# Kernel optimization log

Measured on AMD Instinct MI355X. Metric: run time of the kernel, lower is better.

## Reference

```python
import jax, jax.numpy as jnp
import numpy as np

HEADS = 8
DIM_HEAD = 64
QUERY_DIM = 320
INNER = HEADS * DIM_HEAD
B = 1
N = 2304          # 48*48 latent pixels
HS = WS = 48
SCALE = DIM_HEAD ** -0.5
ATTN_MATRIX_SCALE = 1.5   # injection_config['T']


def setup_inputs() -> dict:
    key = jax.random.key(0)
    ks = jax.random.split(key, 10)
    f = lambda k, s: jax.random.normal(k, s, dtype=jnp.float32)
    return {
        'x': f(ks[0], (B, N, QUERY_DIM)),
        'Wq': f(ks[1], (QUERY_DIM, INNER)) * 0.05,
        'Wo': f(ks[2], (INNER, QUERY_DIM)) * 0.05,
        'bo': jnp.zeros((QUERY_DIM,), jnp.float32),
        'q_injected': f(ks[3], (B * HEADS, N, DIM_HEAD)),
        'k_injected': f(ks[4], (B * HEADS, N, DIM_HEAD)),
        'v_injected': f(ks[5], (B * HEADS, N, DIM_HEAD)),
        'cnt_k_injected': f(ks[6], (B * HEADS, N, DIM_HEAD)),
        'cnt_v_injected': f(ks[7], (B * HEADS, N, DIM_HEAD)),
        'mask': jax.random.uniform(ks[8], (HS, WS), dtype=jnp.float32),
    }


def _split_heads(t):
    # 'b n (h d) -> (b h) n d'
    b, n, _ = t.shape
    return t.reshape(b, n, HEADS, DIM_HEAD).transpose(0, 2, 1, 3).reshape(b * HEADS, n, DIM_HEAD)


def reference(x, Wq, Wo, bo, q_injected, k_injected, v_injected,
              cnt_k_injected, cnt_v_injected, mask):
    # --- q/k/v with injection (b=1 so torch.cat([.]*b) is identity) ---
    q_in = q_injected                          # (bh, N, d)
    q_ = _split_heads(x @ Wq)                  # to_q(x) -> (bh, N, d)
    q = 0.5 * q_in + 0.5 * q_                  # blended query
    k = k_injected
    v = v_injected
    q_cnt, k_cnt, v_cnt = q_in, cnt_k_injected, cnt_v_injected

    # --- get_batch_sim: content-content similarity (b=1 => rearrange is identity) ---
    cc_sim = jnp.einsum('hid,hjd->hij', q_cnt, k_cnt) * SCALE     # (h, N, N)

    # --- get_batch_sim_with_mask ---
    sim = jnp.einsum('hid,hjd->hij', q, k) * (ATTN_MATRIX_SCALE * SCALE)  # (h, N, N)
    sim_r = sim.reshape(HEADS, HS, WS, N)
    cc_r = cc_sim.reshape(HEADS, HS, WS, N)
    max_sim = jnp.einsum('hid,hjd->hij', q_cnt, k)                # delta_q x delta_k (=self.k)
    max_sim_r = max_sim.reshape(HEADS, HS, WS, N)
    min_cc = jnp.min(cc_r, axis=3, keepdims=True)                 # (h, HS, WS, 1)
    max_ms = jnp.max(max_sim_r, axis=3, keepdims=True)            # (h, HS, WS, 1)

    # binary-threshold the mask, flip sign, bilinear-resize to (HS, WS)
    m = jnp.where(mask < 0.5, -1.0, jnp.where(mask > 0.5, 1.0, mask)) * -1.0
    m = jax.image.resize(m[None, None], (1, 1, HS, WS), method='bilinear')
    m = m.reshape(1, HS, WS, 1)

    gvm = (min_cc - max_ms) * m                                   # gradual_vanished_mask
    sim = (sim_r + gvm).reshape(HEADS, N, N)                      # rows [:WS] == all rows here

    # B=1 => the view/permute/reshape block is identity: sim, cc_sim are (h, N, N)
    # concatenated softmax over style keys and content keys
    cat_sim = jnp.concatenate([sim, cc_sim], axis=2)              # (h, N, 2N)
    cat_attn = jax.nn.softmax(cat_sim, axis=-1)
    cat_v = jnp.concatenate([v, v_cnt], axis=1)                   # (h, 2N, d)
    cat_out = jnp.einsum('hij,hjd->hid', cat_attn, cat_v)         # (h, N, d)

    # 'h (b n) d -> b n (h d)' with b=1
    out = cat_out.transpose(1, 0, 2).reshape(B, N, INNER)
    return out @ Wo + bo
```

## Files before the change

### kernel.cpp

```cpp
#include <hip/hip_runtime.h>
#include <math.h>

#define HEADS 8
#define NTOK  2304
#define DH    64
#define QD    320
#define INNER 512
#define NSPLIT 4
#define TPS   18
#define PSTR  68

typedef _Float16 f16;
typedef f16  f16x4 __attribute__((ext_vector_type(4)));
typedef f16  f16x8 __attribute__((ext_vector_type(8)));
typedef float f32x4 __attribute__((ext_vector_type(4)));

#define MFMA(a,b,c) __builtin_amdgcn_mfma_f32_16x16x32_f16((a),(b),(c),0,0,0)

#define GLDS(gp, lp) __builtin_amdgcn_global_load_lds(                      \
    (const __attribute__((address_space(1))) void*)(gp),                    \
    (__attribute__((address_space(3))) void*)(lp), 16, 0, 0)

#if __has_builtin(__builtin_amdgcn_exp2f)
#define EXP2(x) __builtin_amdgcn_exp2f(x)
#else
#define EXP2(x) exp2f(x)
#endif

#define LOG2E 1.44269504f

static __device__ __forceinline__ unsigned pkrtz(float a, float b) {
#if __has_builtin(__builtin_amdgcn_cvt_pkrtz)
  return __builtin_bit_cast(unsigned, __builtin_amdgcn_cvt_pkrtz(a, b));
#else
  union { f16 h[2]; unsigned u; } c;
  c.h[0] = (f16)a; c.h[1] = (f16)b;
  return c.u;
#endif
}

__global__ __launch_bounds__(256) void prep_all(
    const float* __restrict__ qi, const float* __restrict__ ki,
    const float* __restrict__ kc, const float* __restrict__ x,
    const float* __restrict__ v,  const float* __restrict__ vc,
    const float* __restrict__ Wq, const float* __restrict__ Wo,
    f16* __restrict__ oq, f16* __restrict__ ok, f16* __restrict__ okc,
    f16* __restrict__ ox, f16* __restrict__ vt, f16* __restrict__ vct,
    f16* __restrict__ WqT, f16* __restrict__ WoT)
{
  __shared__ float T[64][65];
  const int bid = blockIdx.x;
  const int tid = threadIdx.x;

  if (bid < 2088) {
    int i = bid * 256 + tid;
    const float* src; f16* dst; float s = 1.0f; int off;
    if (i < 147456)      { src = qi; dst = oq;  off = i; }
    else if (i < 294912) { src = ki; dst = ok;  off = i - 147456; }
    else if (i < 442368) { src = kc; dst = okc; off = i - 294912; s = 0.125f * LOG2E; }
    else                 { src = x;  dst = ox;  off = i - 442368; }
    float4 a = reinterpret_cast<const float4*>(src)[off * 2];
    float4 b = reinterpret_cast<const float4*>(src)[off * 2 + 1];
    f16x8 o;
    o[0] = (f16)(a.x * s); o[1] = (f16)(a.y * s);
    o[2] = (f16)(a.z * s); o[3] = (f16)(a.w * s);
    o[4] = (f16)(b.x * s); o[5] = (f16)(b.y * s);
    o[6] = (f16)(b.z * s); o[7] = (f16)(b.w * s);
    *reinterpret_cast<f16x8*>(&dst[(size_t)off * 8]) = o;
  } else if (bid < 2664) {
    int t = bid - 2088;
    int z = t / 288, rem = t % 288;
    int h = rem / 36, nt = rem % 36;
    const float* src = z ? vc : v;
    f16* dst = z ? vct : vt;
    const int n0 = nt * 64;
    const size_t base = ((size_t)h * NTOK + n0) * DH;
    for (int it = 0; it < 4; ++it) {
      int idx = tid + it * 256;
      int n = idx >> 4, d0 = (idx & 15) * 4;
      float4 a = *reinterpret_cast<const float4*>(&src[base + (size_t)n * DH + d0]);
      T[n][d0] = a.x; T[n][d0 + 1] = a.y; T[n][d0 + 2] = a.z; T[n][d0 + 3] = a.w;
    }
    __syncthreads();
    for (int it = 0; it < 2; ++it) {
      int idx = tid + it * 256;
      int d = idx >> 3, c0 = (idx & 7) * 8;
      f16x8 o;
      #pragma unroll
      for (int i = 0; i < 8; ++i) o[i] = (f16)T[c0 + i][d];
      *reinterpret_cast<f16x8*>(&dst[(size_t)(h * 64 + d) * NTOK + n0 + c0]) = o;
    }
  } else {
    int t = bid - 2664;
    int z = t / 40, b = t % 40;
    const float* src = z ? Wo : Wq;
    f16* dst = z ? WoT : WqT;
    const int R = z ? INNER : QD;
    const int C = z ? QD : INNER;
    const int ctiles = C >> 6;
    const int rt = b / ctiles, ct = b % ctiles;
    for (int it = 0; it < 4; ++it) {
      int idx = tid + it * 256;
      int r = idx >> 4, c4 = (idx & 15) * 4;
      float4 a = *reinterpret_cast<const float4*>(&src[(size_t)(rt * 64 + r) * C + ct * 64 + c4]);
      T[r][c4] = a.x; T[r][c4 + 1] = a.y; T[r][c4 + 2] = a.z; T[r][c4 + 3] = a.w;
    }
    __syncthreads();
    for (int it = 0; it < 4; ++it) {
      int idx = tid + it * 256;
      int c = idx >> 4, r4 = (idx & 15) * 4;
      f16x4 o;
      #pragma unroll
      for (int i = 0; i < 4; ++i) o[i] = (f16)T[r4 + i][c];
      *reinterpret_cast<f16x4*>(&dst[(size_t)(ct * 64 + c) * R + rt * 64 + r4]) = o;
    }
  }
}

__global__ __launch_bounds__(256) void qblend_mfma(
    const f16* __restrict__ x16, const f16* __restrict__ WqT,
    const float* __restrict__ qinj, f16* __restrict__ qhat)
{
  const int qt = blockIdx.x, h = blockIdx.y;
  const int n0 = qt * 32;
  const int tid = threadIdx.x;
  const int w = tid >> 6, l = tid & 63, lq = l & 15, lk = l >> 4;
  const int qsub = w & 1, ch = w >> 1;
  f32x4 acc[2] = {};
  const f16* arow = x16 + (size_t)(n0 + qsub * 16 + lq) * QD;
  #pragma unroll
  for (int ks = 0; ks < 10; ++ks) {
    f16x8 a = *reinterpret_cast<const f16x8*>(&arow[ks * 32 + lk * 8]);
    #pragma unroll
    for (int df = 0; df < 2; ++df) {
      const f16* brow = WqT + (size_t)(h * 64 + ch * 32 + df * 16 + lq) * QD;
      f16x8 b = *reinterpret_cast<const f16x8*>(&brow[ks * 32 + lk * 8]);
      acc[df] = MFMA(a, b, acc[df]);
    }
  }
  const float sc = 0.09375f * LOG2E;
  #pragma unroll
  for (int df = 0; df < 2; ++df)
    #pragma unroll
    for (int r = 0; r < 4; ++r) {
      int n = n0 + qsub * 16 + lk * 4 + r;
      int d = ch * 32 + df * 16 + lq;
      size_t idx = ((size_t)h * NTOK + n) * DH + d;
      qhat[idx] = (f16)(sc * (qinj[idx] + acc[df][r]));
    }
}

__global__ __launch_bounds__(128, 2) void attn_nx4(
    const f16* __restrict__ qhat, const f16* __restrict__ qc16,
    const f16* __restrict__ k16,  const f16* __restrict__ kc16,
    const f16* __restrict__ vt16, const f16* __restrict__ vct16,
    float* __restrict__ part)
{
  __shared__ __align__(16) f16 smem[2][2][2048];
  __shared__ __align__(16) f16 pbuf[2][640];

  const int bid = blockIdx.x;
  const int h    = bid & 7;
  const int strm = (bid >> 3) & 1;
  const int sp   = (bid >> 4) & 3;
  const int qt   = bid >> 6;
  const int tid = threadIdx.x;
  const int w = tid >> 6, l = tid & 63;
  const int lq = l & 15, lk = l >> 4;
  const size_t hb = (size_t)h * NTOK * DH;
  const int row0 = qt * 96 + w * 48 + lq;

  f16x8 qh0[2], qh1[2], qh2[2], qc0[2], qc1[2], qc2[2];
  {
    const size_t qr0 = hb + (size_t)row0 * DH;
    #pragma unroll
    for (int ks = 0; ks < 2; ++ks) {
      const int o = ks * 32 + lk * 8;
      qc0[ks] = *reinterpret_cast<const f16x8*>(&qc16[qr0 + o]);
      qc1[ks] = *reinterpret_cast<const f16x8*>(&qc16[qr0 + 16 * DH + o]);
      qc2[ks] = *reinterpret_cast<const f16x8*>(&qc16[qr0 + 32 * DH + o]);
      if (!strm) {
        qh0[ks] = *reinterpret_cast<const f16x8*>(&qhat[qr0 + o]);
        qh1[ks] = *reinterpret_cast<const f16x8*>(&qhat[qr0 + 16 * DH + o]);
        qh2[ks] = *reinterpret_cast<const f16x8*>(&qhat[qr0 + 32 * DH + o]);
      } else { qh0[ks] = qc0[ks]; qh1[ks] = qc1[ks]; qh2[ks] = qc2[ks]; }
    }
  }

  const int krow = tid >> 3;
  const int ksw  = ((tid & 7) ^ (krow & 7)) * 8;
  const int vrow = tid >> 2;
  const int voff = (tid & 3) * 8;
  const f16* gK = (strm ? kc16 : k16) + hb;
  const f16* gV = (strm ? vct16 : vt16) + (size_t)h * DH * NTOK;
  const int lb0 = __builtin_amdgcn_readfirstlane((tid & 64) * 8);
  const int lb1 = 1024 + lb0;

  #define STAGE(nb, j0)                                                      \
    do {                                                                     \
      GLDS(gK + (size_t)((j0) + krow) * 64 + ksw,        &smem[nb][0][lb0]); \
      GLDS(gK + (size_t)((j0) + 16 + krow) * 64 + ksw,   &smem[nb][0][lb1]); \
      GLDS(gV + (size_t)vrow * NTOK + (j0) + voff,       &smem[nb][1][lb0]); \
      GLDS(gV + (size_t)(32 + vrow) * NTOK + (j0) + voff,&smem[nb][1][lb1]); \
    } while (0)

  const int swz = (lq & 7) * 8;
  int xo[2];
  #pragma unroll
  for (int ks = 0; ks < 2; ++ks) xo[ks] = ((ks * 32 + lk * 8) ^ swz);

  float S0 = 0.f, S1 = 0.f, S2 = 0.f;
  float ax0, ax1, ax2;
  ax0 = ax1 = ax2 = strm ? INFINITY : -INFINITY;
  f32x4 O0[4] = {}, O1_[4] = {}, O2_[4] = {};
  f16* Pq = &pbuf[w][0];

  auto SMX = [&](const f32x4* s, float& Sl) -> f16x8 {
    float p0 = EXP2(s[0][0]), p1 = EXP2(s[0][1]);
    float p2 = EXP2(s[0][2]), p3 = EXP2(s[0][3]);
    float p4 = EXP2(s[1][0]), p5 = EXP2(s[1][1]);
    float p6 = EXP2(s[1][2]), p7 = EXP2(s[1][3]);
    Sl += ((p0 + p1) + (p2 + p3)) + ((p4 + p5) + (p6 + p7));
    uint2 wA, wB;
    wA.x = pkrtz(p0, p1); wA.y = pkrtz(p2, p3);
    wB.x = pkrtz(p4, p5); wB.y = pkrtz(p6, p7);
    *reinterpret_cast<uint2*>(Pq + lq * 40 + lk * 4)      = wA;
    *reinterpret_cast<uint2*>(Pq + lq * 40 + 16 + lk * 4) = wB;
    return *reinterpret_cast<const f16x8*>(Pq + lq * 40 + lk * 8);
  };

  const int jb = sp * (TPS * 32);
  STAGE(0, jb);
  asm volatile("s_waitcnt vmcnt(0)" ::: "memory");
  __builtin_amdgcn_sched_barrier(0);
  __builtin_amdgcn_s_barrier();
  __builtin_amdgcn_sched_barrier(0);

  int cur = 0;
  for (int t = 0; t < TPS; ++t) {
    if (t + 1 < TPS) STAGE(cur ^ 1, jb + (t + 1) * 32);

    const f16* Kb = &smem[cur][0][0];
    const f16* Vb = &smem[cur][1][0];

    f32x4 sA[2] = {}, sB[2] = {}, sC[2] = {};
    __builtin_amdgcn_s_setprio(1);
    if (!strm) {
      float m3A = -INFINITY, m3B = -INFINITY, m3C = -INFINITY;
      #pragma unroll
      for (int jf = 0; jf < 2; ++jf) {
        f32x4 tA = {}, tB = {}, tC = {};
        const int rb = (jf * 16 + lq) * 64;
        #pragma unroll
        for (int ks = 0; ks < 2; ++ks) {
          f16x8 aK = *reinterpret_cast<const f16x8*>(&Kb[rb + xo[ks]]);
          sA[jf] = MFMA(aK, qh0[ks], sA[jf]);
          sB[jf] = MFMA(aK, qh1[ks], sB[jf]);
          sC[jf] = MFMA(aK, qh2[ks], sC[jf]);
          tA = MFMA(aK, qc0[ks], tA);
          tB = MFMA(aK, qc1[ks], tB);
          tC = MFMA(aK, qc2[ks], tC);
        }
        m3A = fmaxf(m3A, fmaxf(fmaxf(tA[0], tA[1]), fmaxf(tA[2], tA[3])));
        m3B = fmaxf(m3B, fmaxf(fmaxf(tB[0], tB[1]), fmaxf(tB[2], tB[3])));
        m3C = fmaxf(m3C, fmaxf(fmaxf(tC[0], tC[1]), fmaxf(tC[2], tC[3])));
      }
      ax0 = fmaxf(ax0, m3A); ax1 = fmaxf(ax1, m3B); ax2 = fmaxf(ax2, m3C);
    } else {
      #pragma unroll
      for (int jf = 0; jf < 2; ++jf) {
        const int rb = (jf * 16 + lq) * 64;
        #pragma unroll
        for (int ks = 0; ks < 2; ++ks) {
          f16x8 aK = *reinterpret_cast<const f16x8*>(&Kb[rb + xo[ks]]);
          sA[jf] = MFMA(aK, qc0[ks], sA[jf]);
          sB[jf] = MFMA(aK, qc1[ks], sB[jf]);
          sC[jf] = MFMA(aK, qc2[ks], sC[jf]);
        }
      }
      ax0 = fminf(ax0, fminf(fminf(fminf(sA[0][0], sA[0][1]), fminf(sA[0][2], sA[0][3])),
                             fminf(fminf(sA[1][0], sA[1][1]), fminf(sA[1][2], sA[1][3]))));
      ax1 = fminf(ax1, fminf(fminf(fminf(sB[0][0], sB[0][1]), fminf(sB[0][2], sB[0][3])),
                             fminf(fminf(sB[1][0], sB[1][1]), fminf(sB[1][2], sB[1][3]))));
      ax2 = fminf(ax2, fminf(fminf(fminf(sC[0][0], sC[0][1]), fminf(sC[0][2], sC[0][3])),
                             fminf(fminf(sC[1][0], sC[1][1]), fminf(sC[1][2], sC[1][3]))));
    }
    __builtin_amdgcn_s_setprio(0);

    f16x8 pbA = SMX(sA, S0);
    f16x8 pbB = SMX(sB, S1);
    f16x8 pbC = SMX(sC, S2);

    __builtin_amdgcn_s_setprio(1);
    #pragma unroll
    for (int df = 0; df < 4; ++df) {
      f16x8 aV = *reinterpret_cast<const f16x8*>(&Vb[(df * 16 + lq) * 32 + lk * 8]);
      O0[df]  = MFMA(aV, pbA, O0[df]);
      O1_[df] = MFMA(aV, pbB, O1_[df]);
      O2_[df] = MFMA(aV, pbC, O2_[df]);
    }
    __builtin_amdgcn_s_setprio(0);

    asm volatile("s_waitcnt vmcnt(0)" ::: "memory");
    __builtin_amdgcn_sched_barrier(0);
    __builtin_amdgcn_s_barrier();
    __builtin_amdgcn_sched_barrier(0);
    cur ^= 1;
  }

  S0 += __shfl_xor(S0, 16); S0 += __shfl_xor(S0, 32);
  S1 += __shfl_xor(S1, 16); S1 += __shfl_xor(S1, 32);
  S2 += __shfl_xor(S2, 16); S2 += __shfl_xor(S2, 32);
  if (!strm) {
    ax0 = fmaxf(ax0, __shfl_xor(ax0, 16)); ax0 = fmaxf(ax0, __shfl_xor(ax0, 32));
    ax1 = fmaxf(ax1, __shfl_xor(ax1, 16)); ax1 = fmaxf(ax1, __shfl_xor(ax1, 32));
    ax2 = fmaxf(ax2, __shfl_xor(ax2, 16)); ax2 = fmaxf(ax2, __shfl_xor(ax2, 32));
  } else {
    ax0 = fminf(ax0, __shfl_xor(ax0, 16)); ax0 = fminf(ax0, __shfl_xor(ax0, 32));
    ax1 = fminf(ax1, __shfl_xor(ax1, 16)); ax1 = fminf(ax1, __shfl_xor(ax1, 32));
    ax2 = fminf(ax2, __shfl_xor(ax2, 16)); ax2 = fminf(ax2, __shfl_xor(ax2, 32));
  }
  {
    const size_t u = (size_t)((strm * NSPLIT + sp) * 8 + h);
    float* p0 = part + (u * NTOK + (size_t)row0) * PSTR;
    float* p1 = p0 + (size_t)16 * PSTR;
    float* p2 = p0 + (size_t)32 * PSTR;
    #pragma unroll
    for (int df = 0; df < 4; ++df) {
      *reinterpret_cast<f32x4*>(p0 + df * 16 + lk * 4) = O0[df];
      *reinterpret_cast<f32x4*>(p1 + df * 16 + lk * 4) = O1_[df];
      *reinterpret_cast<f32x4*>(p2 + df * 16 + lk * 4) = O2_[df];
    }
    if (lk == 0) {
      p0[64] = S0; p0[65] = ax0;
      p1[64] = S1; p1[65] = ax1;
      p2[64] = S2; p2[65] = ax2;
    }
  }
  #undef STAGE
}

__global__ __launch_bounds__(256) void merge8(
    const float* __restrict__ part, const float* __restrict__ mask,
    f16* __restrict__ mid)
{
  const int qt = blockIdx.x, h = blockIdx.y;
  const int tid = threadIdx.x;
  const int r = tid >> 2, ds = (tid & 3) * 16;
  const int n = qt * 64 + r;
  const float* pA[NSPLIT];
  const float* pB[NSPLIT];
  #pragma unroll
  for (int s = 0; s < NSPLIT; ++s) {
    pA[s] = part + ((size_t)((0 * NSPLIT + s) * 8 + h) * NTOK + n) * PSTR;
    pB[s] = part + ((size_t)((1 * NSPLIT + s) * 8 + h) * NTOK + n) * PSTR;
  }

  float S1 = 0.f, S2 = 0.f, mx = -INFINITY, mn = INFINITY;
  #pragma unroll
  for (int s = 0; s < NSPLIT; ++s) {
    S1 += pA[s][64]; mx = fmaxf(mx, pA[s][65]);
    S2 += pB[s][64]; mn = fminf(mn, pB[s][65]);
  }

  float mv = mask[n];
  float mm = (mv < 0.5f) ? 1.0f : (mv > 0.5f ? -1.0f : -mv);
  float gvm = (mn - mx * LOG2E) * mm;
  float A1 = gvm;
  float Mf = fmaxf(A1, 0.0f);
  float w1 = exp2f(A1 - Mf), w2 = exp2f(-Mf);
  float inv = 1.0f / (w1 * S1 + w2 * S2);

  f16 ov[16];
  #pragma unroll
  for (int c = 0; c < 4; ++c) {
    float o1[4] = {}, o2[4] = {};
    #pragma unroll
    for (int s = 0; s < NSPLIT; ++s) {
      float4 a = *reinterpret_cast<const float4*>(pA[s] + ds + c * 4);
      float4 b = *reinterpret_cast<const float4*>(pB[s] + ds + c * 4);
      o1[0] += a.x; o1[1] += a.y; o1[2] += a.z; o1[3] += a.w;
      o2[0] += b.x; o2[1] += b.y; o2[2] += b.z; o2[3] += b.w;
    }
    #pragma unroll
    for (int j = 0; j < 4; ++j)
      ov[c * 4 + j] = (f16)((w1 * o1[j] + w2 * o2[j]) * inv);
  }
  f16* dst = mid + (size_t)n * INNER + h * 64 + ds;
  *reinterpret_cast<f16x8*>(dst)     = *reinterpret_cast<f16x8*>(&ov[0]);
  *reinterpret_cast<f16x8*>(dst + 8) = *reinterpret_cast<f16x8*>(&ov[8]);
}

__global__ __launch_bounds__(64) void out_mfma(
    const f16* __restrict__ mid, const f16* __restrict__ WoT,
    const float* __restrict__ bo, float* __restrict__ out)
{
  const int n0 = blockIdx.x * 16;
  const int o0 = blockIdx.y * 64;
  const int l = threadIdx.x, lq = l & 15, lk = l >> 4;
  f32x4 acc[4] = {};
  const f16* arow = mid + (size_t)(n0 + lq) * INNER;
  #pragma unroll
  for (int ks = 0; ks < 16; ++ks) {
    f16x8 a = *reinterpret_cast<const f16x8*>(&arow[ks * 32 + lk * 8]);
    #pragma unroll
    for (int df = 0; df < 4; ++df) {
      f16x8 b = *reinterpret_cast<const f16x8*>(
          &WoT[(size_t)(o0 + df * 16 + lq) * INNER + ks * 32 + lk * 8]);
      acc[df] = MFMA(a, b, acc[df]);
    }
  }
  #pragma unroll
  for (int df = 0; df < 4; ++df) {
    float bb = bo[o0 + df * 16 + lq];
    #pragma unroll
    for (int r = 0; r < 4; ++r) {
      int n = n0 + lk * 4 + r;
      out[(size_t)n * QD + o0 + df * 16 + lq] = acc[df][r] + bb;
    }
  }
}

extern "C" void kernel_launch(void* const* d_in, const int* in_sizes, int n_in,
                              void* d_out, int out_size, void* d_ws, size_t ws_size,
                              hipStream_t stream) {
  const float* x    = (const float*)d_in[0];
  const float* Wq   = (const float*)d_in[1];
  const float* Wo   = (const float*)d_in[2];
  const float* bo   = (const float*)d_in[3];
  const float* qinj = (const float*)d_in[4];
  const float* kinj = (const float*)d_in[5];
  const float* vinj = (const float*)d_in[6];
  const float* kcnt = (const float*)d_in[7];
  const float* vcnt = (const float*)d_in[8];
  const float* mask = (const float*)d_in[9];
  float* out = (float*)d_out;

  const size_t T = (size_t)HEADS * NTOK * DH;
  f16* qhat = (f16*)d_ws;
  f16* qc16 = qhat + T;
  f16* k16  = qc16 + T;
  f16* kc16 = k16  + T;
  f16* vt16 = kc16 + T;
  f16* vct16= vt16 + T;
  f16* mid  = vct16 + T;
  f16* x16  = mid;
  f16* WqT  = mid + 737280;
  f16* WoT  = mid + T;
  float* part = (float*)(WoT + 163840);

  prep_all   <<<2744, 256, 0, stream>>>(qinj, kinj, kcnt, x, vinj, vcnt, Wq, Wo,
                                        qc16, k16, kc16, x16, vt16, vct16, WqT, WoT);
  qblend_mfma<<<dim3(72, 8), 256, 0, stream>>>(x16, WqT, qinj, qhat);
  attn_nx4   <<<1536, 128, 0, stream>>>(qhat, qc16, k16, kc16, vt16, vct16, part);
  merge8     <<<dim3(36, 8), 256, 0, stream>>>(part, mask, mid);
  out_mfma   <<<dim3(144, 5), 64, 0, stream>>>(mid, WoT, bo, out);
}
```

Baseline: 87.63 us.

## Merge key-split pairs inside attention block via LDS, halve partials

Each attention block now has four waves: two query halves times two key splits. The two key-split waves combine their O, S and extremum partials through shared memory before writing, so only two global splits per stream remain. This cuts partial-buffer traffic and the merge kernel's reads. In exchange it adds block-level syncs and larger LDS use, and it changes occupancy through launch_bounds(256,3).

```diff
diff --git a/kernel.cpp b/kernel.cpp
--- a/kernel.cpp
+++ b/kernel.cpp
@@ -6,7 +6,6 @@
 #define DH    64
 #define QD    320
 #define INNER 512
-#define NSPLIT 4
 #define TPS   18
 #define PSTR  68
 
@@ -150,25 +149,26 @@
     }
 }
 
-__global__ __launch_bounds__(128, 2) void attn_nx4(
+__global__ __launch_bounds__(256, 3) void attn_pp(
     const f16* __restrict__ qhat, const f16* __restrict__ qc16,
     const f16* __restrict__ k16,  const f16* __restrict__ kc16,
     const f16* __restrict__ vt16, const f16* __restrict__ vct16,
     float* __restrict__ part)
 {
-  __shared__ __align__(16) f16 smem[2][2][2048];
-  __shared__ __align__(16) f16 pbuf[2][640];
+  __shared__ __align__(16) f16 smemF[2][2][2][2048];
+  __shared__ __align__(16) f16 pbuf[4][640];
 
   const int bid = blockIdx.x;
   const int h    = bid & 7;
   const int strm = (bid >> 3) & 1;
-  const int sp   = (bid >> 4) & 3;
-  const int qt   = bid >> 6;
+  const int spo  = (bid >> 4) & 1;
+  const int qt   = bid >> 5;
   const int tid = threadIdx.x;
   const int w = tid >> 6, l = tid & 63;
   const int lq = l & 15, lk = l >> 4;
+  const int qh = w & 1, spi = w >> 1;
   const size_t hb = (size_t)h * NTOK * DH;
-  const int row0 = qt * 96 + w * 48 + lq;
+  const int row0 = qt * 96 + qh * 48 + lq;
 
   f16x8 qh0[2], qh1[2], qh2[2], qc0[2], qc1[2], qc2[2];
   {
@@ -187,10 +187,11 @@
     }
   }
 
-  const int krow = tid >> 3;
-  const int ksw  = ((tid & 7) ^ (krow & 7)) * 8;
-  const int vrow = tid >> 2;
-  const int voff = (tid & 3) * 8;
+  const int tg = tid & 127;
+  const int krow = tg >> 3;
+  const int ksw  = ((tg & 7) ^ (krow & 7)) * 8;
+  const int vrow = tg >> 2;
+  const int voff = (tg & 3) * 8;
   const f16* gK = (strm ? kc16 : k16) + hb;
   const f16* gV = (strm ? vct16 : vt16) + (size_t)h * DH * NTOK;
   const int lb0 = __builtin_amdgcn_readfirstlane((tid & 64) * 8);
@@ -198,10 +199,12 @@
 
   #define STAGE(nb, j0)                                                      \
     do {                                                                     \
-      GLDS(gK + (size_t)((j0) + krow) * 64 + ksw,        &smem[nb][0][lb0]); \
-      GLDS(gK + (size_t)((j0) + 16 + krow) * 64 + ksw,   &smem[nb][0][lb1]); \
-      GLDS(gV + (size_t)vrow * NTOK + (j0) + voff,       &smem[nb][1][lb0]); \
-      GLDS(gV + (size_t)(32 + vrow) * NTOK + (j0) + voff,&smem[nb][1][lb1]); \
+      GLDS(gK + (size_t)((j0) + krow) * 64 + ksw,  &smemF[spi][nb][0][lb0]); \
+      GLDS(gK + (size_t)((j0) + 16 + krow) * 64 + ksw,                       \
+           &smemF[spi][nb][0][lb1]);                                         \
+      GLDS(gV + (size_t)vrow * NTOK + (j0) + voff, &smemF[spi][nb][1][lb0]); \
+      GLDS(gV + (size_t)(32 + vrow) * NTOK + (j0) + voff,                    \
+           &smemF[spi][nb][1][lb1]);                                         \
     } while (0)
 
   const int swz = (lq & 7) * 8;
@@ -229,7 +232,7 @@
     return *reinterpret_cast<const f16x8*>(Pq + lq * 40 + lk * 8);
   };
 
-  const int jb = sp * (TPS * 32);
+  const int jb = (spo * 2 + spi) * (TPS * 32);
   STAGE(0, jb);
   asm volatile("s_waitcnt vmcnt(0)" ::: "memory");
   __builtin_amdgcn_sched_barrier(0);
@@ -240,8 +243,8 @@
   for (int t = 0; t < TPS; ++t) {
     if (t + 1 < TPS) STAGE(cur ^ 1, jb + (t + 1) * 32);
 
-    const f16* Kb = &smem[cur][0][0];
-    const f16* Vb = &smem[cur][1][0];
+    const f16* Kb = &smemF[spi][cur][0][0];
+    const f16* Vb = &smemF[spi][cur][1][0];
 
     f32x4 sA[2] = {}, sB[2] = {}, sC[2] = {};
     __builtin_amdgcn_s_setprio(1);
@@ -308,20 +311,50 @@
     cur ^= 1;
   }
 
-  S0 += __shfl_xor(S0, 16); S0 += __shfl_xor(S0, 32);
-  S1 += __shfl_xor(S1, 16); S1 += __shfl_xor(S1, 32);
-  S2 += __shfl_xor(S2, 16); S2 += __shfl_xor(S2, 32);
-  if (!strm) {
-    ax0 = fmaxf(ax0, __shfl_xor(ax0, 16)); ax0 = fmaxf(ax0, __shfl_xor(ax0, 32));
-    ax1 = fmaxf(ax1, __shfl_xor(ax1, 16)); ax1 = fmaxf(ax1, __shfl_xor(ax1, 32));
-    ax2 = fmaxf(ax2, __shfl_xor(ax2, 16)); ax2 = fmaxf(ax2, __shfl_xor(ax2, 32));
-  } else {
-    ax0 = fminf(ax0, __shfl_xor(ax0, 16)); ax0 = fminf(ax0, __shfl_xor(ax0, 32));
-    ax1 = fminf(ax1, __shfl_xor(ax1, 16)); ax1 = fminf(ax1, __shfl_xor(ax1, 32));
-    ax2 = fminf(ax2, __shfl_xor(ax2, 16)); ax2 = fminf(ax2, __shfl_xor(ax2, 32));
-  }
-  {
-    const size_t u = (size_t)((strm * NSPLIT + sp) * 8 + h);
+  float* mrg = reinterpret_cast<float*>(&smemF[0][0][0][0]);
+  const int slot = qh * 64 + l;
+  __syncthreads();
+  if (spi == 1) {
+    float* ob = mrg + slot * 48;
+    #pragma unroll
+    for (int df = 0; df < 4; ++df) {
+      *reinterpret_cast<f32x4*>(ob + df * 4)      = O0[df];
+      *reinterpret_cast<f32x4*>(ob + 16 + df * 4) = O1_[df];
+      *reinterpret_cast<f32x4*>(ob + 32 + df * 4) = O2_[df];
+    }
+    float* sb = mrg + 6144 + slot * 6;
+    sb[0] = S0; sb[1] = S1; sb[2] = S2;
+    sb[3] = ax0; sb[4] = ax1; sb[5] = ax2;
+  }
+  __syncthreads();
+  if (spi == 0) {
+    const float* ob = mrg + slot * 48;
+    #pragma unroll
+    for (int df = 0; df < 4; ++df) {
+      O0[df]  += *reinterpret_cast<const f32x4*>(ob + df * 4);
+      O1_[df] += *reinterpret_cast<const f32x4*>(ob + 16 + df * 4);
+      O2_[df] += *reinterpret_cast<const f32x4*>(ob + 32 + df * 4);
+    }
+    const float* sb = mrg + 6144 + slot * 6;
+    S0 += sb[0]; S1 += sb[1]; S2 += sb[2];
+    if (!strm) {
+      ax0 = fmaxf(ax0, sb[3]); ax1 = fmaxf(ax1, sb[4]); ax2 = fmaxf(ax2, sb[5]);
+    } else {
+      ax0 = fminf(ax0, sb[3]); ax1 = fminf(ax1, sb[4]); ax2 = fminf(ax2, sb[5]);
+    }
+    S0 += __shfl_xor(S0, 16); S0 += __shfl_xor(S0, 32);
+    S1 += __shfl_xor(S1, 16); S1 += __shfl_xor(S1, 32);
+    S2 += __shfl_xor(S2, 16); S2 += __shfl_xor(S2, 32);
+    if (!strm) {
+      ax0 = fmaxf(ax0, __shfl_xor(ax0, 16)); ax0 = fmaxf(ax0, __shfl_xor(ax0, 32));
+      ax1 = fmaxf(ax1, __shfl_xor(ax1, 16)); ax1 = fmaxf(ax1, __shfl_xor(ax1, 32));
+      ax2 = fmaxf(ax2, __shfl_xor(ax2, 16)); ax2 = fmaxf(ax2, __shfl_xor(ax2, 32));
+    } else {
+      ax0 = fminf(ax0, __shfl_xor(ax0, 16)); ax0 = fminf(ax0, __shfl_xor(ax0, 32));
+      ax1 = fminf(ax1, __shfl_xor(ax1, 16)); ax1 = fminf(ax1, __shfl_xor(ax1, 32));
+      ax2 = fminf(ax2, __shfl_xor(ax2, 16)); ax2 = fminf(ax2, __shfl_xor(ax2, 32));
+    }
+    const size_t u = (size_t)((strm * 2 + spo) * 8 + h);
     float* p0 = part + (u * NTOK + (size_t)row0) * PSTR;
     float* p1 = p0 + (size_t)16 * PSTR;
     float* p2 = p0 + (size_t)32 * PSTR;
@@ -340,7 +373,7 @@
   #undef STAGE
 }
 
-__global__ __launch_bounds__(256) void merge8(
+__global__ __launch_bounds__(256) void merge4s(
     const float* __restrict__ part, const float* __restrict__ mask,
     f16* __restrict__ mid)
 {
@@ -348,17 +381,17 @@
   const int tid = threadIdx.x;
   const int r = tid >> 2, ds = (tid & 3) * 16;
   const int n = qt * 64 + r;
-  const float* pA[NSPLIT];
-  const float* pB[NSPLIT];
-  #pragma unroll
-  for (int s = 0; s < NSPLIT; ++s) {
-    pA[s] = part + ((size_t)((0 * NSPLIT + s) * 8 + h) * NTOK + n) * PSTR;
-    pB[s] = part + ((size_t)((1 * NSPLIT + s) * 8 + h) * NTOK + n) * PSTR;
+  const float* pA[2];
+  const float* pB[2];
+  #pragma unroll
+  for (int s = 0; s < 2; ++s) {
+    pA[s] = part + ((size_t)((0 * 2 + s) * 8 + h) * NTOK + n) * PSTR;
+    pB[s] = part + ((size_t)((1 * 2 + s) * 8 + h) * NTOK + n) * PSTR;
   }
 
   float S1 = 0.f, S2 = 0.f, mx = -INFINITY, mn = INFINITY;
   #pragma unroll
-  for (int s = 0; s < NSPLIT; ++s) {
+  for (int s = 0; s < 2; ++s) {
     S1 += pA[s][64]; mx = fmaxf(mx, pA[s][65]);
     S2 += pB[s][64]; mn = fminf(mn, pB[s][65]);
   }
@@ -376,7 +409,7 @@
   for (int c = 0; c < 4; ++c) {
     float o1[4] = {}, o2[4] = {};
     #pragma unroll
-    for (int s = 0; s < NSPLIT; ++s) {
+    for (int s = 0; s < 2; ++s) {
       float4 a = *reinterpret_cast<const float4*>(pA[s] + ds + c * 4);
       float4 b = *reinterpret_cast<const float4*>(pB[s] + ds + c * 4);
       o1[0] += a.x; o1[1] += a.y; o1[2] += a.z; o1[3] += a.w;
@@ -452,7 +485,7 @@
   prep_all   <<<2744, 256, 0, stream>>>(qinj, kinj, kcnt, x, vinj, vcnt, Wq, Wo,
                                         qc16, k16, kc16, x16, vt16, vct16, WqT, WoT);
   qblend_mfma<<<dim3(72, 8), 256, 0, stream>>>(x16, WqT, qinj, qhat);
-  attn_nx4   <<<1536, 128, 0, stream>>>(qhat, qc16, k16, kc16, vt16, vct16, part);
-  merge8     <<<dim3(36, 8), 256, 0, stream>>>(part, mask, mid);
+  attn_pp    <<<768, 256, 0, stream>>>(qhat, qc16, k16, kc16, vt16, vct16, part);
+  merge4s    <<<dim3(36, 8), 256, 0, stream>>>(part, mask, mid);
   out_mfma   <<<dim3(144, 5), 64, 0, stream>>>(mid, WoT, bo, out);
 }
```

After: 82.81 us. 5.5% less time.
